# Kernel optimization log

Hardware: AMD Instinct MI355X
Metric: run time of the kernel (lower is better)

## Reference

```python
import jax, jax.numpy as jnp
import numpy as np

N = 200000   # nodes (Elliptic-scale)
E = 500000   # directed edges
F = 166      # in_channels / node feature dim
H = 128      # hidden_channels
C = 2        # out_channels
T = 49       # number of time steps


def setup_inputs() -> dict:
    key = jax.random.key(0)
    ks = jax.random.split(key, 12)
    x = jax.random.normal(ks[0], (N, F), jnp.float32)
    edge_index = jax.random.randint(ks[1], (2, E), 0, N, dtype=jnp.int32)
    time_step = jax.random.randint(ks[2], (N,), 0, T, dtype=jnp.int32)
    sF = 1.0 / np.sqrt(F)
    sH = 1.0 / np.sqrt(H)
    initial_w = jax.random.uniform(ks[3], (F, F), jnp.float32, -sF, sF)
    gru_w_ih = jax.random.uniform(ks[4], (3 * F, F), jnp.float32, -sF, sF)
    gru_w_hh = jax.random.uniform(ks[5], (3 * F, F), jnp.float32, -sF, sF)
    gru_b_ih = jax.random.uniform(ks[6], (3 * F,), jnp.float32, -sF, sF)
    gru_b_hh = jax.random.uniform(ks[7], (3 * F,), jnp.float32, -sF, sF)
    proj_w = jax.random.uniform(ks[8], (H, F), jnp.float32, -sF, sF)
    proj_b = jax.random.uniform(ks[9], (H,), jnp.float32, -sF, sF)
    cls_w = jax.random.uniform(ks[10], (C, H), jnp.float32, -sH, sH)
    cls_b = jax.random.uniform(ks[11], (C,), jnp.float32, -sH, sH)
    return {"x": x, "edge_index": edge_index, "time_step": time_step,
            "initial_w": initial_w, "gru_w_ih": gru_w_ih, "gru_w_hh": gru_w_hh,
            "gru_b_ih": gru_b_ih, "gru_b_hh": gru_b_hh,
            "proj_w": proj_w, "proj_b": proj_b, "cls_w": cls_w, "cls_b": cls_b}


def reference(x, edge_index, time_step, initial_w, gru_w_ih, gru_w_hh,
              gru_b_ih, gru_b_hh, proj_w, proj_b, cls_w, cls_b):
    src, dst = edge_index[0], edge_index[1]
    n = x.shape[0]

    def gru(W):
        # torch.nn.GRU single step, input = hidden = W  (FxF matrix, rows = batch)
        gi = W @ gru_w_ih.T + gru_b_ih
        gh = W @ gru_w_hh.T + gru_b_hh
        i_r, i_z, i_n = jnp.split(gi, 3, axis=-1)
        h_r, h_z, h_n = jnp.split(gh, 3, axis=-1)
        r = jax.nn.sigmoid(i_r + h_r)
        z = jax.nn.sigmoid(i_z + h_z)
        nn_ = jnp.tanh(i_n + r * h_n)
        return (1.0 - z) * nn_ + z * W

    def step(carry, t):
        W, logits = carry
        W = gru(W)  # evolve GCN weight (EvolveGCN-O)
        # subgraph of nodes with time_step <= t, expressed by masking (same math
        # as relabel+extract: inactive nodes contribute nothing, their outputs are ignored)
        act = time_step <= t
        ew = (act[src] & act[dst]).astype(x.dtype)
        # gcn_norm with self-loops: deg = in-degree over active edges + 1
        deg = jax.ops.segment_sum(ew, dst, num_segments=n) + 1.0
        dinv = jax.lax.rsqrt(deg)
        norm = ew * dinv[src] * dinv[dst]
        h = jnp.where(act[:, None], x, 0.0) @ W               # [N, F]
        agg = jax.ops.segment_sum(h[src] * norm[:, None], dst, num_segments=n)
        agg = agg + h / deg[:, None]                          # self-loop term dinv_i^2 * h_i
        z = jax.nn.relu(agg @ proj_w.T + proj_b)              # [N, H] (dropout: eval mode)
        lg = z @ cls_w.T + cls_b                              # [N, C]
        logits = jnp.where((time_step == t)[:, None], lg, logits)
        return (W, logits), None

    init = (initial_w, jnp.zeros((n, cls_w.shape[0]), x.dtype))
    (_, logits), _ = jax.lax.scan(step, init, jnp.arange(T, dtype=time_step.dtype))
    return logits
```

## Files before the change

### kernel.cpp

```cpp
#include <hip/hip_runtime.h>
#include <hip/hip_fp16.h>
#include <math.h>

#define NN 200000
#define NE 500000
#define FF 166
#define HH 128
#define CC 2
#define TT 49
#define GG 498
#define PADN 203136
#define MAXTILES 6400
#define KP 84
#define KPAD 192
#define SCB 512
#define SNB 391
#define HB 782
#define PREPB 420
#define CIB 1954
#define XSB 37500

typedef _Float16 half2v __attribute__((ext_vector_type(2)));
typedef _Float16 f16x4 __attribute__((ext_vector_type(4)));
typedef _Float16 f16x8 __attribute__((ext_vector_type(8)));
typedef float f32x4 __attribute__((ext_vector_type(4)));

static __device__ __forceinline__ float fdot2f(half2v a, half2v b, float c) {
#if __has_builtin(__builtin_amdgcn_fdot2)
    return __builtin_amdgcn_fdot2(a, b, c, false);
#else
    return c + (float)a.x * (float)b.x + (float)a.y * (float)b.y;
#endif
}

__global__ __launch_bounds__(256) void setup1(
        const float* __restrict__ wih, const float* __restrict__ whh,
        const float* __restrict__ projw,
        _Float16* __restrict__ wkp, float* __restrict__ projwT,
        const int* __restrict__ dstp, int* __restrict__ offc,
        const int* __restrict__ ts, int* __restrict__ cnt, int* __restrict__ rank) {
    __shared__ int h[64];
    int b = blockIdx.x;
    int tid = threadIdx.x;
    if (b < PREPB) {
        int idx = b * 256 + tid;
        const int A = 2 * KP * 512;
        if (idx < A) {
            int m = idx / (KP * 512);
            int r = idx - m * (KP * 512);
            int kp = r >> 9, c = r & 511;
            const float* Wm = m ? whh : wih;
            float x0 = 0.0f, x1 = 0.0f;
            if (c < GG) {
                int k0 = 2 * kp, k1 = 2 * kp + 1;
                if (k0 < FF) x0 = Wm[c * FF + k0];
                if (k1 < FF) x1 = Wm[c * FF + k1];
            }
            wkp[2 * idx]     = (_Float16)x0;
            wkp[2 * idx + 1] = (_Float16)x1;
        } else if (idx < A + FF * HH) {
            int q = idx - A;
            int k = q >> 7, hh = q & 127;
            projwT[q] = projw[hh * FF + k];
        }
    } else if (b < PREPB + CIB) {
        int e = (b - PREPB) * 256 + tid;
        if (e < NE) atomicAdd(&offc[dstp[e]], 1);
    } else {
        int hb = b - PREPB - CIB;
        if (tid < TT) h[tid] = 0;
        __syncthreads();
        int i = hb * 256 + tid;
        if (i < NN) {
            int t = ts[i];
            rank[i] = atomicAdd(&h[t], 1);
        }
        __syncthreads();
        if (tid < TT) cnt[hb * TT + tid] = h[tid];
    }
}

__global__ __launch_bounds__(256) void setup2(
        const int* __restrict__ off, int* __restrict__ bsum,
        const int* __restrict__ cnt, int* __restrict__ basecol, int* __restrict__ bcnt) {
    __shared__ int s[256];
    int b = blockIdx.x, tid = threadIdx.x;
    if (b < SNB) {
        int i0 = b * SCB + tid * 2;
        int v = 0;
        if (i0 < NN) v += off[i0];
        if (i0 + 1 < NN) v += off[i0 + 1];
        s[tid] = v;
        __syncthreads();
        for (int d = 128; d > 0; d >>= 1) {
            if (tid < d) s[tid] += s[tid + d];
            __syncthreads();
        }
        if (tid == 0) bsum[b] = s[0];
    } else {
        int t = b - SNB;
        const int CH = (HB + 255) / 256;
        int b0 = tid * CH;
        int loc[4];
        int sum = 0;
        for (int u = 0; u < CH; ++u) {
            int bb = b0 + u;
            int v = (bb < HB) ? cnt[bb * TT + t] : 0;
            loc[u] = sum;
            sum += v;
        }
        s[tid] = sum;
        __syncthreads();
        for (int d = 1; d < 256; d <<= 1) {
            int u = (tid >= d) ? s[tid - d] : 0;
            __syncthreads();
            s[tid] += u;
            __syncthreads();
        }
        int base = s[tid] - sum;
        for (int u = 0; u < CH; ++u) {
            int bb = b0 + u;
            if (bb < HB) basecol[bb * TT + t] = base + loc[u];
        }
        if (tid == 255) bcnt[t] = s[255];
    }
}

__global__ __launch_bounds__(512) void setup3(
        const int* __restrict__ bsum, int* __restrict__ bpre, int* __restrict__ off,
        const int* __restrict__ bcnt, int* __restrict__ pstart,
        int* __restrict__ tile_t, int* __restrict__ tile_r0, int* __restrict__ meta) {
    __shared__ int s[512];
    int tid = threadIdx.x;
    if (blockIdx.x == 0) {
        int v = (tid < SNB) ? bsum[tid] : 0;
        s[tid] = v;
        __syncthreads();
        for (int d = 1; d < 512; d <<= 1) {
            int u = (tid >= d) ? s[tid - d] : 0;
            __syncthreads();
            s[tid] += u;
            __syncthreads();
        }
        bpre[tid] = s[tid] - v;
        if (tid == 511) off[NN] = s[511];
    } else {
        int t = tid;
        int nt = (t < TT) ? (bcnt[t] + 31) / 32 : 0;
        if (t < 64) s[t] = nt;
        __syncthreads();
        for (int d = 1; d < 64; d <<= 1) {
            int v = (t >= d && t < 64) ? s[t - d] : 0;
            __syncthreads();
            if (t < 64) s[t] += v;
            __syncthreads();
        }
        if (t < 64) {
            int ntbase = s[t] - nt;
            int pbase = ntbase * 32;
            if (t < TT) {
                pstart[t] = pbase;
                for (int u = 0; u < nt; ++u) {
                    tile_t[ntbase + u] = t;
                    tile_r0[ntbase + u] = pbase + u * 32;
                }
            }
            if (t == 63) {
                meta[0] = s[63];
                meta[1] = s[63] * 32;
                pstart[TT] = s[63] * 32;
            }
        }
    }
}

__global__ __launch_bounds__(512) void setup4(
        int* __restrict__ off, const int* __restrict__ bpre,
        const int* __restrict__ ts, const int* __restrict__ rank,
        const int* __restrict__ basecol, const int* __restrict__ pstart,
        int* __restrict__ perm, int* __restrict__ pos) {
    __shared__ int s[512];
    int b = blockIdx.x, tid = threadIdx.x;
    if (b < SNB) {
        int i = b * SCB + tid;
        int v = (i < NN) ? off[i] : 0;
        s[tid] = v;
        __syncthreads();
        for (int d = 1; d < 512; d <<= 1) {
            int u = (tid >= d) ? s[tid - d] : 0;
            __syncthreads();
            s[tid] += u;
            __syncthreads();
        }
        if (i < NN) off[i] = s[tid] - v + bpre[b];
    } else {
        int i = (b - SNB) * 512 + tid;
        if (i < NN) {
            int t = ts[i];
            int hb = i >> 8;
            int p = pstart[t] + basecol[hb * TT + t] + rank[i];
            perm[p] = i;
            pos[i] = p;
        }
    }
}

__global__ __launch_bounds__(256) void setup5(
        const int* __restrict__ srcp, const int* __restrict__ dstp,
        const int* __restrict__ ts, const int* __restrict__ off,
        int* __restrict__ cursor, int2* __restrict__ adjst,
        const float* __restrict__ x, const int* __restrict__ pos,
        f16x4* __restrict__ x2p4) {
    int b = blockIdx.x, tid = threadIdx.x;
    if (b < CIB) {
        int e = b * 256 + tid;
        if (e < NE) {
            int d = dstp[e];
            int s2 = srcp[e];
            int p = atomicAdd(&cursor[d], 1);
            adjst[off[d] + p] = make_int2(s2, ts[s2]);
        }
    } else {
        int idx = (b - CIB) * 256 + tid;
        if (idx >= NN * 48) return;
        int i = idx / 48, cp4 = idx - i * 48;
        int c0 = cp4 * 4;
        float v0 = 0.f, v1 = 0.f, v2 = 0.f, v3 = 0.f;
        const float* xr = x + (size_t)i * FF;
        if (c0 + 3 < FF) {
            float2 p0 = *(const float2*)(xr + c0);
            float2 p1 = *(const float2*)(xr + c0 + 2);
            v0 = p0.x; v1 = p0.y; v2 = p1.x; v3 = p1.y;
        } else if (c0 < FF) {
            float2 p0 = *(const float2*)(xr + c0);
            v0 = p0.x; v1 = p0.y;
        }
        f16x4 h;
        h[0] = (_Float16)v0; h[1] = (_Float16)v1;
        h[2] = (_Float16)v2; h[3] = (_Float16)v3;
        x2p4[(size_t)pos[i] * 48 + cp4] = h;
    }
}

__global__ __launch_bounds__(256) void degf_hist(const int* __restrict__ off, const int2* __restrict__ adjst,
                                                 const int* __restrict__ ts, _Float16* __restrict__ dinvh,
                                                 float* __restrict__ selfdeg) {
    __shared__ unsigned short sh[TT * 256];
    int tid = threadIdx.x;
    int i = blockIdx.x * 256 + tid;
    for (int t = 0; t < TT; ++t) sh[t * 256 + tid] = 0;
    if (i >= NN) return;
    int tsi = ts[i];
    int e0 = off[i], e1 = off[i + 1];
    for (int e = e0; e < e1; ++e) {
        int tj = adjst[e].y;
        sh[tj * 256 + tid]++;
    }
    int cum = 1;
    for (int t = 0; t < TT; ++t) {
        cum += sh[t * 256 + tid];
        dinvh[(size_t)t * NN + i] = (_Float16)rsqrtf((float)cum);
        if (t == tsi) selfdeg[i] = 1.0f / (float)cum;
    }
}

__global__ __launch_bounds__(256) void edge_compact(
        const int* __restrict__ off, const int2* __restrict__ adjst,
        const int* __restrict__ ts, const _Float16* __restrict__ dinvh, const int* __restrict__ pos,
        int2* __restrict__ ewp, int* __restrict__ nact) {
    int i = blockIdx.x * 256 + threadIdx.x;
    if (i >= NN) return;
    int t = ts[i];
    const _Float16* dv = dinvh + (size_t)t * NN;
    float dvi = (float)dv[i];
    int e0 = off[i], e1 = off[i + 1];
    int c = e0;
    for (int e = e0; e < e1; ++e) {
        int2 a = adjst[e];
        if (a.y <= t) {
            float w = (float)dv[a.x] * dvi;
            ewp[c++] = make_int2(pos[a.x], __float_as_int(w));
        }
    }
    nact[i] = c - e0;
}

__global__ __launch_bounds__(512) void gru_evolve(
        const float* __restrict__ initial_w,
        const _Float16* __restrict__ wkp,
        const float* __restrict__ bih, const float* __restrict__ bhh,
        float* __restrict__ W_all) {
    __shared__ float s_w[FF];
    __shared__ __align__(16) _Float16 s_wh[2 * KP];
    __shared__ float s_pre[2][512];
    int tid = threadIdx.x;
    int row = blockIdx.x;

    if (tid < FF) {
        float v = initial_w[(size_t)row * FF + tid];
        s_w[tid] = v;
        s_wh[tid] = (_Float16)v;
    } else if (tid < 2 * KP) {
        s_wh[tid] = (_Float16)0.0f;
    }

    int cc0 = tid * 2;
    bool act = cc0 < 996;
    int m = (cc0 >= 498) ? 1 : 0;
    int c0 = act ? (cc0 - m * 498) : 0;

    half2v wr0[KP], wr1[KP];
    {
        const half2v* __restrict__ pW =
            (const half2v*)wkp + (size_t)(act ? m : 0) * (KP * 512) + c0;
        #pragma unroll
        for (int kp = 0; kp < KP; ++kp) {
            wr0[kp] = pW[(size_t)(kp << 9)];
            wr1[kp] = pW[(size_t)(kp << 9) + 1];
        }
    }

    float bi_r = 0, bi_z = 0, bi_n = 0, bh_r = 0, bh_z = 0, bh_n = 0;
    if (tid < FF) {
        bi_r = bih[tid]; bi_z = bih[FF + tid]; bi_n = bih[2 * FF + tid];
        bh_r = bhh[tid]; bh_z = bhh[FF + tid]; bh_n = bhh[2 * FF + tid];
    }
    __syncthreads();

    const f16x8* s_wh8 = (const f16x8*)s_wh;
    for (int t = 0; t < TT; ++t) {
        if (act) {
            float a0 = 0.0f, a1 = 0.0f;
            #pragma unroll
            for (int q = 0; q < 21; ++q) {
                f16x8 w8 = s_wh8[q];
                half2v h0 = __builtin_shufflevector(w8, w8, 0, 1);
                half2v h1 = __builtin_shufflevector(w8, w8, 2, 3);
                half2v h2 = __builtin_shufflevector(w8, w8, 4, 5);
                half2v h3 = __builtin_shufflevector(w8, w8, 6, 7);
                a0 = fdot2f(wr0[4 * q + 0], h0, a0);  a1 = fdot2f(wr1[4 * q + 0], h0, a1);
                a0 = fdot2f(wr0[4 * q + 1], h1, a0);  a1 = fdot2f(wr1[4 * q + 1], h1, a1);
                a0 = fdot2f(wr0[4 * q + 2], h2, a0);  a1 = fdot2f(wr1[4 * q + 2], h2, a1);
                a0 = fdot2f(wr0[4 * q + 3], h3, a0);  a1 = fdot2f(wr1[4 * q + 3], h3, a1);
            }
            s_pre[m][c0]     = a0;
            s_pre[m][c0 + 1] = a1;
        }
        __syncthreads();
        if (tid < FF) {
            float i_r = s_pre[0][tid]          + bi_r;
            float h_r = s_pre[1][tid]          + bh_r;
            float i_z = s_pre[0][FF + tid]     + bi_z;
            float h_z = s_pre[1][FF + tid]     + bh_z;
            float i_n = s_pre[0][2 * FF + tid] + bi_n;
            float h_n = s_pre[1][2 * FF + tid] + bh_n;
            float rg = 1.0f / (1.0f + expf(-(i_r + h_r)));
            float zg = 1.0f / (1.0f + expf(-(i_z + h_z)));
            float ng = tanhf(i_n + rg * h_n);
            float wnew = (1.0f - zg) * ng + zg * s_w[tid];
            s_w[tid] = wnew;
            s_wh[tid] = (_Float16)wnew;
            W_all[((size_t)t * FF + row) * FF + tid] = wnew;
        }
        __syncthreads();
    }
}

__global__ __launch_bounds__(1024) void m_build(const float* __restrict__ W_all,
                                                const float* __restrict__ projwT,
                                                _Float16* __restrict__ Mh) {
    __shared__ __align__(16) float sw[8][168];
    int blk = blockIdx.x;
    int t = blk / 24, rb = blk - t * 24;
    int tid = threadIdx.x;
    int r0 = rb * 8;
    for (int idx = tid; idx < 8 * FF; idx += 1024) {
        int rr = idx / FF, k = idx - rr * FF;
        int r = r0 + rr;
        sw[rr][k] = (r < FF) ? W_all[((size_t)t * FF + r) * FF + k] : 0.0f;
    }
    __syncthreads();
    int rr = tid >> 7, h = tid & 127;
    int r = r0 + rr;
    if (r >= KPAD) return;
    float acc = 0.0f;
    if (r < FF) {
        const float* __restrict__ pw = projwT + h;
        #pragma unroll 4
        for (int c4 = 0; c4 < 164; c4 += 4) {
            float4 w = *(const float4*)&sw[rr][c4];
            acc += w.x * pw[(size_t)(c4 + 0) << 7];
            acc += w.y * pw[(size_t)(c4 + 1) << 7];
            acc += w.z * pw[(size_t)(c4 + 2) << 7];
            acc += w.w * pw[(size_t)(c4 + 3) << 7];
        }
        acc += sw[rr][164] * pw[(size_t)164 << 7];
        acc += sw[rr][165] * pw[(size_t)165 << 7];
    }
    Mh[((size_t)t * HH + h) * KPAD + r] = (_Float16)acc;
}

__global__ __launch_bounds__(512) void gemm_fused5(
        const int* __restrict__ meta, const int* __restrict__ tile_t,
        const int* __restrict__ tile_r0, const int* __restrict__ perm,
        const float* __restrict__ selfdeg, const f16x4* __restrict__ x2p4,
        const int* __restrict__ off, const int* __restrict__ nact,
        const int2* __restrict__ ewp,
        const _Float16* __restrict__ Mh, const float* __restrict__ proj_b,
        const float* __restrict__ cls_w, const float* __restrict__ cls_b,
        float* __restrict__ out) {
    __shared__ __align__(16) char smraw[32 * 130 * 4];
    _Float16* sY = (_Float16*)smraw;
    float* sP = (float*)smraw;
    int bid = blockIdx.x;
    if (bid >= meta[0]) return;
    int t = tile_t[bid], r0 = tile_r0[bid];
    int tid = threadIdx.x;
    int lane = tid & 63;
    int w = tid >> 6;
    bool ln48 = lane < 48;

    {
        const uint4* src = (const uint4*)(x2p4 + (size_t)r0 * 48);
        #pragma unroll
        for (int u = 0; u < 2; ++u) {
            int q = tid + u * 512;
            if (q < 768) {
                int row = q / 24, kc = q - row * 24;
                *(uint4*)(sY + row * 200 + kc * 8) = src[q];
            }
        }
    }
    __syncthreads();

    int rbase = w * 4;
    int ep[4], ee[4];
    float ac[4][4];
    #pragma unroll
    for (int q = 0; q < 4; ++q) {
        int r = rbase + q;
        int i = perm[r0 + r];
        float sw = 0.0f;
        ep[q] = 0; ee[q] = 0;
        if (i >= 0) {
            sw = selfdeg[i];
            ep[q] = off[i];
            ee[q] = ep[q] + nact[i];
        }
        f16x4 h = (f16x4)((_Float16)0.0f);
        if (ln48) h = *(const f16x4*)(sY + r * 200 + lane * 4);
        ac[q][0] = sw * (float)h[0];
        ac[q][1] = sw * (float)h[1];
        ac[q][2] = sw * (float)h[2];
        ac[q][3] = sw * (float)h[3];
    }
    int2 pc[4];
    #pragma unroll
    for (int q = 0; q < 4; ++q) pc[q] = (ep[q] < ee[q]) ? ewp[ep[q]] : make_int2(0, 0);
    while ((ep[0] < ee[0]) | (ep[1] < ee[1]) | (ep[2] < ee[2]) | (ep[3] < ee[3])) {
        int js[4]; float wv[4];
        #pragma unroll
        for (int q = 0; q < 4; ++q) {
            bool val = ep[q] < ee[q];
            js[q] = pc[q].x;
            wv[q] = val ? __int_as_float(pc[q].y) : 0.0f;
            if (val) ep[q]++;
        }
        #pragma unroll
        for (int q = 0; q < 4; ++q) pc[q] = (ep[q] < ee[q]) ? ewp[ep[q]] : make_int2(0, 0);
        #pragma unroll
        for (int q = 0; q < 4; ++q) {
            if (wv[q] != 0.0f && ln48) {
                f16x4 g = x2p4[(size_t)js[q] * 48 + lane];
                ac[q][0] += wv[q] * (float)g[0];
                ac[q][1] += wv[q] * (float)g[1];
                ac[q][2] += wv[q] * (float)g[2];
                ac[q][3] += wv[q] * (float)g[3];
            }
        }
    }
    #pragma unroll
    for (int q = 0; q < 4; ++q) {
        if (ln48) {
            f16x4 o;
            o[0] = (_Float16)ac[q][0];
            o[1] = (_Float16)ac[q][1];
            o[2] = (_Float16)ac[q][2];
            o[3] = (_Float16)ac[q][3];
            *(f16x4*)(sY + (rbase + q) * 200 + lane * 4) = o;
        }
    }
    __syncthreads();

    int lr = lane & 15;
    int kg = lane >> 4;
    int c0 = w * 16;
    f32x4 acc0 = {0, 0, 0, 0}, acc1 = {0, 0, 0, 0};
    const _Float16* B0 = Mh + ((size_t)t * HH + c0 + lr) * KPAD + kg * 8;
    const _Float16* A0 = sY + lr * 200 + kg * 8;
    const _Float16* A1 = A0 + 16 * 200;

    #pragma unroll
    for (int s = 0; s < 6; ++s) {
        f16x8 b0 = *(const f16x8*)(B0 + s * 32);
        f16x8 a0 = *(const f16x8*)(A0 + s * 32);
        f16x8 a1 = *(const f16x8*)(A1 + s * 32);
        acc0 = __builtin_amdgcn_mfma_f32_16x16x32_f16(a0, b0, acc0, 0, 0, 0);
        acc1 = __builtin_amdgcn_mfma_f32_16x16x32_f16(a1, b0, acc1, 0, 0, 0);
    }

    float pb = proj_b[c0 + lr];
    __syncthreads();
    int prow = kg * 4;
    int colw = c0 + lr;
    #pragma unroll
    for (int r = 0; r < 4; ++r) {
        sP[(prow + r) * 130 + colw]      = fmaxf(acc0[r] + pb, 0.0f);
        sP[(16 + prow + r) * 130 + colw] = fmaxf(acc1[r] + pb, 0.0f);
    }
    __syncthreads();

    int row = tid >> 4, cc = (tid >> 3) & 1, qq = tid & 7;
    const float* pr = sP + row * 130 + qq * 16;
    const float* cw = cls_w + cc * HH + qq * 16;
    float s = 0.0f;
    #pragma unroll
    for (int h = 0; h < 16; ++h) s += pr[h] * cw[h];
    s += __shfl_xor(s, 1);
    s += __shfl_xor(s, 2);
    s += __shfl_xor(s, 4);
    if (qq == 0) {
        int node = perm[r0 + row];
        if (node >= 0) out[(size_t)node * CC + cc] = s + cls_b[cc];
    }
}

extern "C" void kernel_launch(void* const* d_in, const int* in_sizes, int n_in,
                              void* d_out, int out_size, void* d_ws, size_t ws_size,
                              hipStream_t stream) {
    const float* x = (const float*)d_in[0];
    const int* ei = (const int*)d_in[1];
    const int* srcp = ei;
    const int* dstp = ei + NE;
    const int* ts = (const int*)d_in[2];
    const float* initial_w = (const float*)d_in[3];
    const float* wih = (const float*)d_in[4];
    const float* whh = (const float*)d_in[5];
    const float* bih = (const float*)d_in[6];
    const float* bhh = (const float*)d_in[7];
    const float* projw = (const float*)d_in[8];
    const float* projb = (const float*)d_in[9];
    const float* clsw = (const float*)d_in[10];
    const float* clsb = (const float*)d_in[11];
    float* out = (float*)d_out;

    char* base = (char*)d_ws;
    size_t o = 0;
    auto alloc = [&](size_t bytes) { size_t r = o; o = (o + bytes + 255) & ~(size_t)255; return r; };

    float*    W_all   = (float*)   (base + alloc((size_t)TT * FF * FF * 4));
    _Float16* Mh      = (_Float16*)(base + alloc((size_t)TT * HH * KPAD * 2));
    _Float16* wkp     = (_Float16*)(base + alloc((size_t)2 * KP * 512 * 2 * 2));
    float*    projwT  = (float*)   (base + alloc((size_t)FF * HH * 4));
    int*      off     = (int*)     (base + alloc((size_t)(NN + 1) * 4));
    int*      cursor  = (int*)     (base + alloc((size_t)NN * 4));
    int2*     adjst   = (int2*)    (base + alloc((size_t)NE * 8));
    int2*     ewp     = (int2*)    (base + alloc((size_t)NE * 8));
    _Float16* dinvh   = (_Float16*)(base + alloc((size_t)TT * NN * 2));
    float*    selfdeg = (float*)   (base + alloc((size_t)NN * 4));
    int*      nact    = (int*)     (base + alloc((size_t)NN * 4));
    int*      pos     = (int*)     (base + alloc((size_t)NN * 4));
    int*      bcnt    = (int*)     (base + alloc((size_t)TT * 4));
    int*      pstart  = (int*)     (base + alloc((size_t)(TT + 1) * 4));
    int*      meta    = (int*)     (base + alloc(2 * 4));
    int*      tile_t  = (int*)     (base + alloc((size_t)MAXTILES * 4));
    int*      tile_r0 = (int*)     (base + alloc((size_t)MAXTILES * 4));
    int*      perm    = (int*)     (base + alloc((size_t)PADN * 4));
    int*      bsum    = (int*)     (base + alloc((size_t)512 * 4));
    int*      bpre    = (int*)     (base + alloc((size_t)520 * 4));
    int*      cnt     = (int*)     (base + alloc((size_t)HB * TT * 4));
    int*      basecol = (int*)     (base + alloc((size_t)HB * TT * 4));
    int*      rank    = (int*)     (base + alloc((size_t)NN * 4));
    f16x4*    x2p4    = (f16x4*)   (base + alloc((size_t)PADN * 48 * 8));

    hipMemsetAsync(off, 0, (size_t)((char*)cursor - (char*)off) + (size_t)NN * 4, stream);
    hipMemsetAsync(perm, 0xFF, (size_t)PADN * 4, stream);

    setup1<<<PREPB + CIB + HB, 256, 0, stream>>>(wih, whh, projw, wkp, projwT,
                                                 dstp, off, ts, cnt, rank);
    setup2<<<SNB + TT, 256, 0, stream>>>(off, bsum, cnt, basecol, bcnt);
    setup3<<<2, 512, 0, stream>>>(bsum, bpre, off, bcnt, pstart, tile_t, tile_r0, meta);
    setup4<<<SNB + SNB, 512, 0, stream>>>(off, bpre, ts, rank, basecol, pstart, perm, pos);
    setup5<<<CIB + XSB, 256, 0, stream>>>(srcp, dstp, ts, off, cursor, adjst, x, pos, x2p4);
    degf_hist<<<(NN + 255) / 256, 256, 0, stream>>>(off, adjst, ts, dinvh, selfdeg);
    edge_compact<<<(NN + 255) / 256, 256, 0, stream>>>(off, adjst, ts, dinvh, pos, ewp, nact);

    gru_evolve<<<FF, 512, 0, stream>>>(initial_w, wkp, bih, bhh, W_all);
    m_build<<<TT * 24, 1024, 0, stream>>>(W_all, projwT, Mh);

    gemm_fused5<<<MAXTILES, 512, 0, stream>>>(meta, tile_t, tile_r0, perm, selfdeg,
                                              x2p4, off, nact, ewp, Mh, projb, clsw, clsb, out);
}
```

Before: 334.4 us.

## Merge degree histogram with M build, pack pos into adjacency, halve GEMM block width

Several changes land at once. The degree histogram kernel and the M=W·projW build kernel are fused into one launch, and gru_evolve moves earlier in the stream. Each adjacency entry now packs the source time step and its permuted position into one int, so edge_compact no longer gathers pos. setup1 now uses 512-thread blocks. The fused GEMM kernel drops from 512 to 256 threads per tile, so each wave handles 8 rows of edge gathering and a 32x32 MFMA output block, and the edge prefetch double-buffering is removed. The goal is fewer launches and less gather traffic, at the cost of lower parallelism per tile and less latency hiding in the gather loop.

```diff
diff --git a/kernel.cpp b/kernel.cpp
--- a/kernel.cpp
+++ b/kernel.cpp
@@ -16,9 +16,13 @@
 #define SCB 512
 #define SNB 391
 #define HB 782
-#define PREPB 420
 #define CIB 1954
 #define XSB 37500
+#define P2B 210
+#define C2B 977
+#define H2B 391
+#define DEGB 782
+#define MBB (TT * 96)
 
 typedef _Float16 half2v __attribute__((ext_vector_type(2)));
 typedef _Float16 f16x4 __attribute__((ext_vector_type(4)));
@@ -33,17 +37,17 @@
 #endif
 }
 
-__global__ __launch_bounds__(256) void setup1(
+__global__ __launch_bounds__(512) void setup1(
         const float* __restrict__ wih, const float* __restrict__ whh,
         const float* __restrict__ projw,
         _Float16* __restrict__ wkp, float* __restrict__ projwT,
         const int* __restrict__ dstp, int* __restrict__ offc,
         const int* __restrict__ ts, int* __restrict__ cnt, int* __restrict__ rank) {
-    __shared__ int h[64];
+    __shared__ int h2[2][TT];
     int b = blockIdx.x;
     int tid = threadIdx.x;
-    if (b < PREPB) {
-        int idx = b * 256 + tid;
+    if (b < P2B) {
+        int idx = b * 512 + tid;
         const int A = 2 * KP * 512;
         if (idx < A) {
             int m = idx / (KP * 512);
@@ -63,226 +67,23 @@
             int k = q >> 7, hh = q & 127;
             projwT[q] = projw[hh * FF + k];
         }
-    } else if (b < PREPB + CIB) {
-        int e = (b - PREPB) * 256 + tid;
+    } else if (b < P2B + C2B) {
+        int e = (b - P2B) * 512 + tid;
         if (e < NE) atomicAdd(&offc[dstp[e]], 1);
     } else {
-        int hb = b - PREPB - CIB;
-        if (tid < TT) h[tid] = 0;
-        __syncthreads();
-        int i = hb * 256 + tid;
+        int hb2 = b - P2B - C2B;
+        int sub = tid >> 8;
+        int lt = tid & 255;
+        if (lt < TT) h2[sub][lt] = 0;
+        __syncthreads();
+        int i = hb2 * 512 + tid;
         if (i < NN) {
             int t = ts[i];
-            rank[i] = atomicAdd(&h[t], 1);
-        }
-        __syncthreads();
-        if (tid < TT) cnt[hb * TT + tid] = h[tid];
-    }
-}
-
-__global__ __launch_bounds__(256) void setup2(
-        const int* __restrict__ off, int* __restrict__ bsum,
-        const int* __restrict__ cnt, int* __restrict__ basecol, int* __restrict__ bcnt) {
-    __shared__ int s[256];
-    int b = blockIdx.x, tid = threadIdx.x;
-    if (b < SNB) {
-        int i0 = b * SCB + tid * 2;
-        int v = 0;
-        if (i0 < NN) v += off[i0];
-        if (i0 + 1 < NN) v += off[i0 + 1];
-        s[tid] = v;
-        __syncthreads();
-        for (int d = 128; d > 0; d >>= 1) {
-            if (tid < d) s[tid] += s[tid + d];
-            __syncthreads();
-        }
-        if (tid == 0) bsum[b] = s[0];
-    } else {
-        int t = b - SNB;
-        const int CH = (HB + 255) / 256;
-        int b0 = tid * CH;
-        int loc[4];
-        int sum = 0;
-        for (int u = 0; u < CH; ++u) {
-            int bb = b0 + u;
-            int v = (bb < HB) ? cnt[bb * TT + t] : 0;
-            loc[u] = sum;
-            sum += v;
-        }
-        s[tid] = sum;
-        __syncthreads();
-        for (int d = 1; d < 256; d <<= 1) {
-            int u = (tid >= d) ? s[tid - d] : 0;
-            __syncthreads();
-            s[tid] += u;
-            __syncthreads();
-        }
-        int base = s[tid] - sum;
-        for (int u = 0; u < CH; ++u) {
-            int bb = b0 + u;
-            if (bb < HB) basecol[bb * TT + t] = base + loc[u];
-        }
-        if (tid == 255) bcnt[t] = s[255];
-    }
-}
-
-__global__ __launch_bounds__(512) void setup3(
-        const int* __restrict__ bsum, int* __restrict__ bpre, int* __restrict__ off,
-        const int* __restrict__ bcnt, int* __restrict__ pstart,
-        int* __restrict__ tile_t, int* __restrict__ tile_r0, int* __restrict__ meta) {
-    __shared__ int s[512];
-    int tid = threadIdx.x;
-    if (blockIdx.x == 0) {
-        int v = (tid < SNB) ? bsum[tid] : 0;
-        s[tid] = v;
-        __syncthreads();
-        for (int d = 1; d < 512; d <<= 1) {
-            int u = (tid >= d) ? s[tid - d] : 0;
-            __syncthreads();
-            s[tid] += u;
-            __syncthreads();
-        }
-        bpre[tid] = s[tid] - v;
-        if (tid == 511) off[NN] = s[511];
-    } else {
-        int t = tid;
-        int nt = (t < TT) ? (bcnt[t] + 31) / 32 : 0;
-        if (t < 64) s[t] = nt;
-        __syncthreads();
-        for (int d = 1; d < 64; d <<= 1) {
-            int v = (t >= d && t < 64) ? s[t - d] : 0;
-            __syncthreads();
-            if (t < 64) s[t] += v;
-            __syncthreads();
-        }
-        if (t < 64) {
-            int ntbase = s[t] - nt;
-            int pbase = ntbase * 32;
-            if (t < TT) {
-                pstart[t] = pbase;
-                for (int u = 0; u < nt; ++u) {
-                    tile_t[ntbase + u] = t;
-                    tile_r0[ntbase + u] = pbase + u * 32;
-                }
-            }
-            if (t == 63) {
-                meta[0] = s[63];
-                meta[1] = s[63] * 32;
-                pstart[TT] = s[63] * 32;
-            }
-        }
-    }
-}
-
-__global__ __launch_bounds__(512) void setup4(
-        int* __restrict__ off, const int* __restrict__ bpre,
-        const int* __restrict__ ts, const int* __restrict__ rank,
-        const int* __restrict__ basecol, const int* __restrict__ pstart,
-        int* __restrict__ perm, int* __restrict__ pos) {
-    __shared__ int s[512];
-    int b = blockIdx.x, tid = threadIdx.x;
-    if (b < SNB) {
-        int i = b * SCB + tid;
-        int v = (i < NN) ? off[i] : 0;
-        s[tid] = v;
-        __syncthreads();
-        for (int d = 1; d < 512; d <<= 1) {
-            int u = (tid >= d) ? s[tid - d] : 0;
-            __syncthreads();
-            s[tid] += u;
-            __syncthreads();
-        }
-        if (i < NN) off[i] = s[tid] - v + bpre[b];
-    } else {
-        int i = (b - SNB) * 512 + tid;
-        if (i < NN) {
-            int t = ts[i];
-            int hb = i >> 8;
-            int p = pstart[t] + basecol[hb * TT + t] + rank[i];
-            perm[p] = i;
-            pos[i] = p;
-        }
-    }
-}
-
-__global__ __launch_bounds__(256) void setup5(
-        const int* __restrict__ srcp, const int* __restrict__ dstp,
-        const int* __restrict__ ts, const int* __restrict__ off,
-        int* __restrict__ cursor, int2* __restrict__ adjst,
-        const float* __restrict__ x, const int* __restrict__ pos,
-        f16x4* __restrict__ x2p4) {
-    int b = blockIdx.x, tid = threadIdx.x;
-    if (b < CIB) {
-        int e = b * 256 + tid;
-        if (e < NE) {
-            int d = dstp[e];
-            int s2 = srcp[e];
-            int p = atomicAdd(&cursor[d], 1);
-            adjst[off[d] + p] = make_int2(s2, ts[s2]);
-        }
-    } else {
-        int idx = (b - CIB) * 256 + tid;
-        if (idx >= NN * 48) return;
-        int i = idx / 48, cp4 = idx - i * 48;
-        int c0 = cp4 * 4;
-        float v0 = 0.f, v1 = 0.f, v2 = 0.f, v3 = 0.f;
-        const float* xr = x + (size_t)i * FF;
-        if (c0 + 3 < FF) {
-            float2 p0 = *(const float2*)(xr + c0);
-            float2 p1 = *(const float2*)(xr + c0 + 2);
-            v0 = p0.x; v1 = p0.y; v2 = p1.x; v3 = p1.y;
-        } else if (c0 < FF) {
-            float2 p0 = *(const float2*)(xr + c0);
-            v0 = p0.x; v1 = p0.y;
-        }
-        f16x4 h;
-        h[0] = (_Float16)v0; h[1] = (_Float16)v1;
-        h[2] = (_Float16)v2; h[3] = (_Float16)v3;
-        x2p4[(size_t)pos[i] * 48 + cp4] = h;
-    }
-}
-
-__global__ __launch_bounds__(256) void degf_hist(const int* __restrict__ off, const int2* __restrict__ adjst,
-                                                 const int* __restrict__ ts, _Float16* __restrict__ dinvh,
-                                                 float* __restrict__ selfdeg) {
-    __shared__ unsigned short sh[TT * 256];
-    int tid = threadIdx.x;
-    int i = blockIdx.x * 256 + tid;
-    for (int t = 0; t < TT; ++t) sh[t * 256 + tid] = 0;
-    if (i >= NN) return;
-    int tsi = ts[i];
-    int e0 = off[i], e1 = off[i + 1];
-    for (int e = e0; e < e1; ++e) {
-        int tj = adjst[e].y;
-        sh[tj * 256 + tid]++;
-    }
-    int cum = 1;
-    for (int t = 0; t < TT; ++t) {
-        cum += sh[t * 256 + tid];
-        dinvh[(size_t)t * NN + i] = (_Float16)rsqrtf((float)cum);
-        if (t == tsi) selfdeg[i] = 1.0f / (float)cum;
-    }
-}
-
-__global__ __launch_bounds__(256) void edge_compact(
-        const int* __restrict__ off, const int2* __restrict__ adjst,
-        const int* __restrict__ ts, const _Float16* __restrict__ dinvh, const int* __restrict__ pos,
-        int2* __restrict__ ewp, int* __restrict__ nact) {
-    int i = blockIdx.x * 256 + threadIdx.x;
-    if (i >= NN) return;
-    int t = ts[i];
-    const _Float16* dv = dinvh + (size_t)t * NN;
-    float dvi = (float)dv[i];
-    int e0 = off[i], e1 = off[i + 1];
-    int c = e0;
-    for (int e = e0; e < e1; ++e) {
-        int2 a = adjst[e];
-        if (a.y <= t) {
-            float w = (float)dv[a.x] * dvi;
-            ewp[c++] = make_int2(pos[a.x], __float_as_int(w));
-        }
-    }
-    nact[i] = c - e0;
+            rank[i] = atomicAdd(&h2[sub][t], 1);
+        }
+        __syncthreads();
+        if (lt < TT) cnt[(hb2 * 2 + sub) * TT + lt] = h2[sub][lt];
+    }
 }
 
 __global__ __launch_bounds__(512) void gru_evolve(
@@ -366,41 +167,246 @@
     }
 }
 
-__global__ __launch_bounds__(1024) void m_build(const float* __restrict__ W_all,
-                                                const float* __restrict__ projwT,
-                                                _Float16* __restrict__ Mh) {
-    __shared__ __align__(16) float sw[8][168];
-    int blk = blockIdx.x;
-    int t = blk / 24, rb = blk - t * 24;
+__global__ __launch_bounds__(256) void setup2(
+        const int* __restrict__ off, int* __restrict__ bsum,
+        const int* __restrict__ cnt, int* __restrict__ basecol, int* __restrict__ bcnt) {
+    __shared__ int s[256];
+    int b = blockIdx.x, tid = threadIdx.x;
+    if (b < SNB) {
+        int i0 = b * SCB + tid * 2;
+        int v = 0;
+        if (i0 < NN) v += off[i0];
+        if (i0 + 1 < NN) v += off[i0 + 1];
+        s[tid] = v;
+        __syncthreads();
+        for (int d = 128; d > 0; d >>= 1) {
+            if (tid < d) s[tid] += s[tid + d];
+            __syncthreads();
+        }
+        if (tid == 0) bsum[b] = s[0];
+    } else {
+        int t = b - SNB;
+        const int CH = (HB + 255) / 256;
+        int b0 = tid * CH;
+        int loc[4];
+        int sum = 0;
+        for (int u = 0; u < CH; ++u) {
+            int bb = b0 + u;
+            int v = (bb < HB) ? cnt[bb * TT + t] : 0;
+            loc[u] = sum;
+            sum += v;
+        }
+        s[tid] = sum;
+        __syncthreads();
+        for (int d = 1; d < 256; d <<= 1) {
+            int u = (tid >= d) ? s[tid - d] : 0;
+            __syncthreads();
+            s[tid] += u;
+            __syncthreads();
+        }
+        int base = s[tid] - sum;
+        for (int u = 0; u < CH; ++u) {
+            int bb = b0 + u;
+            if (bb < HB) basecol[bb * TT + t] = base + loc[u];
+        }
+        if (tid == 255) bcnt[t] = s[255];
+    }
+}
+
+__global__ __launch_bounds__(512) void setup3(
+        const int* __restrict__ bsum, int* __restrict__ bpre, int* __restrict__ off,
+        const int* __restrict__ bcnt, int* __restrict__ pstart,
+        int* __restrict__ tile_t, int* __restrict__ tile_r0, int* __restrict__ meta) {
+    __shared__ int s[512];
     int tid = threadIdx.x;
-    int r0 = rb * 8;
-    for (int idx = tid; idx < 8 * FF; idx += 1024) {
-        int rr = idx / FF, k = idx - rr * FF;
+    if (blockIdx.x == 0) {
+        int v = (tid < SNB) ? bsum[tid] : 0;
+        s[tid] = v;
+        __syncthreads();
+        for (int d = 1; d < 512; d <<= 1) {
+            int u = (tid >= d) ? s[tid - d] : 0;
+            __syncthreads();
+            s[tid] += u;
+            __syncthreads();
+        }
+        bpre[tid] = s[tid] - v;
+        if (tid == 511) off[NN] = s[511];
+    } else {
+        int t = tid;
+        int nt = (t < TT) ? (bcnt[t] + 31) / 32 : 0;
+        if (t < 64) s[t] = nt;
+        __syncthreads();
+        for (int d = 1; d < 64; d <<= 1) {
+            int v = (t >= d && t < 64) ? s[t - d] : 0;
+            __syncthreads();
+            if (t < 64) s[t] += v;
+            __syncthreads();
+        }
+        if (t < 64) {
+            int ntbase = s[t] - nt;
+            int pbase = ntbase * 32;
+            if (t < TT) {
+                pstart[t] = pbase;
+                for (int u = 0; u < nt; ++u) {
+                    tile_t[ntbase + u] = t;
+                    tile_r0[ntbase + u] = pbase + u * 32;
+                }
+            }
+            if (t == 63) {
+                meta[0] = s[63];
+                meta[1] = s[63] * 32;
+                pstart[TT] = s[63] * 32;
+            }
+        }
+    }
+}
+
+__global__ __launch_bounds__(512) void setup4(
+        int* __restrict__ off, const int* __restrict__ bpre,
+        const int* __restrict__ ts, const int* __restrict__ rank,
+        const int* __restrict__ basecol, const int* __restrict__ pstart,
+        int* __restrict__ perm, int* __restrict__ pos) {
+    __shared__ int s[512];
+    int b = blockIdx.x, tid = threadIdx.x;
+    if (b < SNB) {
+        int i = b * SCB + tid;
+        int v = (i < NN) ? off[i] : 0;
+        s[tid] = v;
+        __syncthreads();
+        for (int d = 1; d < 512; d <<= 1) {
+            int u = (tid >= d) ? s[tid - d] : 0;
+            __syncthreads();
+            s[tid] += u;
+            __syncthreads();
+        }
+        if (i < NN) off[i] = s[tid] - v + bpre[b];
+    } else {
+        int i = (b - SNB) * 512 + tid;
+        if (i < NN) {
+            int t = ts[i];
+            int hb = i >> 8;
+            int p = pstart[t] + basecol[hb * TT + t] + rank[i];
+            perm[p] = i;
+            pos[i] = p;
+        }
+    }
+}
+
+__global__ __launch_bounds__(256) void setup5(
+        const int* __restrict__ srcp, const int* __restrict__ dstp,
+        const int* __restrict__ ts, const int* __restrict__ off,
+        int* __restrict__ cursor, int2* __restrict__ adjst,
+        const float* __restrict__ x, const int* __restrict__ pos,
+        f16x4* __restrict__ x2p4) {
+    int b = blockIdx.x, tid = threadIdx.x;
+    if (b < CIB) {
+        int e = b * 256 + tid;
+        if (e < NE) {
+            int d = dstp[e];
+            int s2 = srcp[e];
+            int p = atomicAdd(&cursor[d], 1);
+            adjst[off[d] + p] = make_int2(s2, (ts[s2] << 25) | pos[s2]);
+        }
+    } else {
+        int idx = (b - CIB) * 256 + tid;
+        if (idx >= NN * 48) return;
+        int i = idx / 48, cp4 = idx - i * 48;
+        int c0 = cp4 * 4;
+        float v0 = 0.f, v1 = 0.f, v2 = 0.f, v3 = 0.f;
+        const float* xr = x + (size_t)i * FF;
+        if (c0 + 3 < FF) {
+            float2 p0 = *(const float2*)(xr + c0);
+            float2 p1 = *(const float2*)(xr + c0 + 2);
+            v0 = p0.x; v1 = p0.y; v2 = p1.x; v3 = p1.y;
+        } else if (c0 < FF) {
+            float2 p0 = *(const float2*)(xr + c0);
+            v0 = p0.x; v1 = p0.y;
+        }
+        f16x4 h;
+        h[0] = (_Float16)v0; h[1] = (_Float16)v1;
+        h[2] = (_Float16)v2; h[3] = (_Float16)v3;
+        x2p4[(size_t)pos[i] * 48 + cp4] = h;
+    }
+}
+
+__global__ __launch_bounds__(256) void degf_m(
+        const int* __restrict__ off, const int2* __restrict__ adjst,
+        const int* __restrict__ ts, _Float16* __restrict__ dinvh,
+        float* __restrict__ selfdeg,
+        const float* __restrict__ W_all, const float* __restrict__ projwT,
+        _Float16* __restrict__ Mh) {
+    __shared__ unsigned short sh[TT * 256];
+    __shared__ __align__(16) float sw2[2][168];
+    int b = blockIdx.x;
+    int tid = threadIdx.x;
+    if (b < DEGB) {
+        int i = b * 256 + tid;
+        for (int t = 0; t < TT; ++t) sh[t * 256 + tid] = 0;
+        if (i >= NN) return;
+        int tsi = ts[i];
+        int e0 = off[i], e1 = off[i + 1];
+        for (int e = e0; e < e1; ++e) {
+            int tj = adjst[e].y >> 25;
+            sh[tj * 256 + tid]++;
+        }
+        int cum = 1;
+        for (int t = 0; t < TT; ++t) {
+            cum += sh[t * 256 + tid];
+            dinvh[(size_t)t * NN + i] = (_Float16)rsqrtf((float)cum);
+            if (t == tsi) selfdeg[i] = 1.0f / (float)cum;
+        }
+    } else {
+        int mb = b - DEGB;
+        int t = mb / 96, rb = mb - t * 96;
+        int r0 = rb * 2;
+        for (int idx = tid; idx < 2 * FF; idx += 256) {
+            int rr = idx / FF, k = idx - rr * FF;
+            int r = r0 + rr;
+            sw2[rr][k] = (r < FF) ? W_all[((size_t)t * FF + r) * FF + k] : 0.0f;
+        }
+        __syncthreads();
+        int rr = tid >> 7, h = tid & 127;
         int r = r0 + rr;
-        sw[rr][k] = (r < FF) ? W_all[((size_t)t * FF + r) * FF + k] : 0.0f;
-    }
-    __syncthreads();
-    int rr = tid >> 7, h = tid & 127;
-    int r = r0 + rr;
-    if (r >= KPAD) return;
-    float acc = 0.0f;
-    if (r < FF) {
-        const float* __restrict__ pw = projwT + h;
-        #pragma unroll 4
-        for (int c4 = 0; c4 < 164; c4 += 4) {
-            float4 w = *(const float4*)&sw[rr][c4];
-            acc += w.x * pw[(size_t)(c4 + 0) << 7];
-            acc += w.y * pw[(size_t)(c4 + 1) << 7];
-            acc += w.z * pw[(size_t)(c4 + 2) << 7];
-            acc += w.w * pw[(size_t)(c4 + 3) << 7];
-        }
-        acc += sw[rr][164] * pw[(size_t)164 << 7];
-        acc += sw[rr][165] * pw[(size_t)165 << 7];
-    }
-    Mh[((size_t)t * HH + h) * KPAD + r] = (_Float16)acc;
-}
-
-__global__ __launch_bounds__(512) void gemm_fused5(
+        float acc = 0.0f;
+        if (r < FF) {
+            const float* __restrict__ pw = projwT + h;
+            #pragma unroll 4
+            for (int c4 = 0; c4 < 164; c4 += 4) {
+                float4 w = *(const float4*)&sw2[rr][c4];
+                acc += w.x * pw[(size_t)(c4 + 0) << 7];
+                acc += w.y * pw[(size_t)(c4 + 1) << 7];
+                acc += w.z * pw[(size_t)(c4 + 2) << 7];
+                acc += w.w * pw[(size_t)(c4 + 3) << 7];
+            }
+            acc += sw2[rr][164] * pw[(size_t)164 << 7];
+            acc += sw2[rr][165] * pw[(size_t)165 << 7];
+        }
+        Mh[((size_t)t * HH + h) * KPAD + r] = (_Float16)acc;
+    }
+}
+
+__global__ __launch_bounds__(256) void edge_compact(
+        const int* __restrict__ off, const int2* __restrict__ adjst,
+        const int* __restrict__ ts, const _Float16* __restrict__ dinvh,
+        int2* __restrict__ ewp, int* __restrict__ nact) {
+    int i = blockIdx.x * 256 + threadIdx.x;
+    if (i >= NN) return;
+    int t = ts[i];
+    const _Float16* dv = dinvh + (size_t)t * NN;
+    float dvi = (float)dv[i];
+    int e0 = off[i], e1 = off[i + 1];
+    int c = e0;
+    for (int e = e0; e < e1; ++e) {
+        int2 a = adjst[e];
+        if ((a.y >> 25) <= t) {
+            float w = (float)dv[a.x] * dvi;
+            ewp[c++] = make_int2(a.y & 0x1FFFFFF, __float_as_int(w));
+        }
+    }
+    nact[i] = c - e0;
+}
+
+__global__ __launch_bounds__(256) void gemm_fused6(
         const int* __restrict__ meta, const int* __restrict__ tile_t,
         const int* __restrict__ tile_r0, const int* __restrict__ perm,
         const float* __restrict__ selfdeg, const f16x4* __restrict__ x2p4,
@@ -423,21 +429,19 @@
     {
         const uint4* src = (const uint4*)(x2p4 + (size_t)r0 * 48);
         #pragma unroll
-        for (int u = 0; u < 2; ++u) {
-            int q = tid + u * 512;
-            if (q < 768) {
-                int row = q / 24, kc = q - row * 24;
-                *(uint4*)(sY + row * 200 + kc * 8) = src[q];
-            }
+        for (int u = 0; u < 3; ++u) {
+            int q = tid + u * 256;
+            int row = q / 24, kc = q - row * 24;
+            *(uint4*)(sY + row * 200 + kc * 8) = src[q];
         }
     }
     __syncthreads();
 
-    int rbase = w * 4;
-    int ep[4], ee[4];
-    float ac[4][4];
+    int rbase = w * 8;
+    int ep[8], ee[8];
+    float ac[8][4];
     #pragma unroll
-    for (int q = 0; q < 4; ++q) {
+    for (int q = 0; q < 8; ++q) {
         int r = rbase + q;
         int i = perm[r0 + r];
         float sw = 0.0f;
@@ -454,22 +458,21 @@
         ac[q][2] = sw * (float)h[2];
         ac[q][3] = sw * (float)h[3];
     }
-    int2 pc[4];
+    bool more = false;
     #pragma unroll
-    for (int q = 0; q < 4; ++q) pc[q] = (ep[q] < ee[q]) ? ewp[ep[q]] : make_int2(0, 0);
-    while ((ep[0] < ee[0]) | (ep[1] < ee[1]) | (ep[2] < ee[2]) | (ep[3] < ee[3])) {
-        int js[4]; float wv[4];
+    for (int q = 0; q < 8; ++q) more |= (ep[q] < ee[q]);
+    while (more) {
+        int js[8]; float wv[8];
         #pragma unroll
-        for (int q = 0; q < 4; ++q) {
-            bool val = ep[q] < ee[q];
-            js[q] = pc[q].x;
-            wv[q] = val ? __int_as_float(pc[q].y) : 0.0f;
-            if (val) ep[q]++;
+        for (int q = 0; q < 8; ++q) {
+            bool v = ep[q] < ee[q];
+            int2 p = v ? ewp[ep[q]] : make_int2(0, 0);
+            js[q] = p.x;
+            wv[q] = v ? __int_as_float(p.y) : 0.0f;
+            if (v) ep[q]++;
         }
         #pragma unroll
-        for (int q = 0; q < 4; ++q) pc[q] = (ep[q] < ee[q]) ? ewp[ep[q]] : make_int2(0, 0);
-        #pragma unroll
-        for (int q = 0; q < 4; ++q) {
+        for (int q = 0; q < 8; ++q) {
             if (wv[q] != 0.0f && ln48) {
                 f16x4 g = x2p4[(size_t)js[q] * 48 + lane];
                 ac[q][0] += wv[q] * (float)g[0];
@@ -478,9 +481,12 @@
                 ac[q][3] += wv[q] * (float)g[3];
             }
         }
+        more = false;
+        #pragma unroll
+        for (int q = 0; q < 8; ++q) more |= (ep[q] < ee[q]);
     }
     #pragma unroll
-    for (int q = 0; q < 4; ++q) {
+    for (int q = 0; q < 8; ++q) {
         if (ln48) {
             f16x4 o;
             o[0] = (_Float16)ac[q][0];
@@ -494,41 +500,46 @@
 
     int lr = lane & 15;
     int kg = lane >> 4;
-    int c0 = w * 16;
-    f32x4 acc0 = {0, 0, 0, 0}, acc1 = {0, 0, 0, 0};
-    const _Float16* B0 = Mh + ((size_t)t * HH + c0 + lr) * KPAD + kg * 8;
+    f32x4 acc00 = {0,0,0,0}, acc01 = {0,0,0,0}, acc10 = {0,0,0,0}, acc11 = {0,0,0,0};
+    const _Float16* B0 = Mh + ((size_t)t * HH + w * 32 + lr) * KPAD + kg * 8;
+    const _Float16* B1 = B0 + 16 * KPAD;
     const _Float16* A0 = sY + lr * 200 + kg * 8;
     const _Float16* A1 = A0 + 16 * 200;
 
     #pragma unroll
     for (int s = 0; s < 6; ++s) {
-        f16x8 b0 = *(const f16x8*)(B0 + s * 32);
         f16x8 a0 = *(const f16x8*)(A0 + s * 32);
         f16x8 a1 = *(const f16x8*)(A1 + s * 32);
-        acc0 = __builtin_amdgcn_mfma_f32_16x16x32_f16(a0, b0, acc0, 0, 0, 0);
-        acc1 = __builtin_amdgcn_mfma_f32_16x16x32_f16(a1, b0, acc1, 0, 0, 0);
-    }
-
-    float pb = proj_b[c0 + lr];
+        f16x8 b0 = *(const f16x8*)(B0 + s * 32);
+        f16x8 b1 = *(const f16x8*)(B1 + s * 32);
+        acc00 = __builtin_amdgcn_mfma_f32_16x16x32_f16(a0, b0, acc00, 0, 0, 0);
+        acc01 = __builtin_amdgcn_mfma_f32_16x16x32_f16(a0, b1, acc01, 0, 0, 0);
+        acc10 = __builtin_amdgcn_mfma_f32_16x16x32_f16(a1, b0, acc10, 0, 0, 0);
+        acc11 = __builtin_amdgcn_mfma_f32_16x16x32_f16(a1, b1, acc11, 0, 0, 0);
+    }
+
+    float pb0 = proj_b[w * 32 + lr];
+    float pb1 = proj_b[w * 32 + 16 + lr];
     __syncthreads();
     int prow = kg * 4;
-    int colw = c0 + lr;
+    int col0 = w * 32 + lr;
     #pragma unroll
     for (int r = 0; r < 4; ++r) {
-        sP[(prow + r) * 130 + colw]      = fmaxf(acc0[r] + pb, 0.0f);
-        sP[(16 + prow + r) * 130 + colw] = fmaxf(acc1[r] + pb, 0.0f);
+        sP[(prow + r) * 130 + col0]           = fmaxf(acc00[r] + pb0, 0.0f);
+        sP[(prow + r) * 130 + col0 + 16]      = fmaxf(acc01[r] + pb1, 0.0f);
+        sP[(16 + prow + r) * 130 + col0]      = fmaxf(acc10[r] + pb0, 0.0f);
+        sP[(16 + prow + r) * 130 + col0 + 16] = fmaxf(acc11[r] + pb1, 0.0f);
     }
     __syncthreads();
 
-    int row = tid >> 4, cc = (tid >> 3) & 1, qq = tid & 7;
-    const float* pr = sP + row * 130 + qq * 16;
-    const float* cw = cls_w + cc * HH + qq * 16;
+    int row = tid >> 3, cc = (tid >> 2) & 1, qq = tid & 3;
+    const float* pr = sP + row * 130 + qq * 32;
+    const float* cw = cls_w + cc * HH + qq * 32;
     float s = 0.0f;
-    #pragma unroll
-    for (int h = 0; h < 16; ++h) s += pr[h] * cw[h];
+    #pragma unroll 8
+    for (int h = 0; h < 32; ++h) s += pr[h] * cw[h];
     s += __shfl_xor(s, 1);
     s += __shfl_xor(s, 2);
-    s += __shfl_xor(s, 4);
     if (qq == 0) {
         int node = perm[r0 + row];
         if (node >= 0) out[(size_t)node * CC + cc] = s + cls_b[cc];
@@ -586,18 +597,16 @@
     hipMemsetAsync(off, 0, (size_t)((char*)cursor - (char*)off) + (size_t)NN * 4, stream);
     hipMemsetAsync(perm, 0xFF, (size_t)PADN * 4, stream);
 
-    setup1<<<PREPB + CIB + HB, 256, 0, stream>>>(wih, whh, projw, wkp, projwT,
-                                                 dstp, off, ts, cnt, rank);
+    setup1<<<P2B + C2B + H2B, 512, 0, stream>>>(wih, whh, projw, wkp, projwT,
+                                                dstp, off, ts, cnt, rank);
+    gru_evolve<<<FF, 512, 0, stream>>>(initial_w, wkp, bih, bhh, W_all);
     setup2<<<SNB + TT, 256, 0, stream>>>(off, bsum, cnt, basecol, bcnt);
     setup3<<<2, 512, 0, stream>>>(bsum, bpre, off, bcnt, pstart, tile_t, tile_r0, meta);
     setup4<<<SNB + SNB, 512, 0, stream>>>(off, bpre, ts, rank, basecol, pstart, perm, pos);
     setup5<<<CIB + XSB, 256, 0, stream>>>(srcp, dstp, ts, off, cursor, adjst, x, pos, x2p4);
-    degf_hist<<<(NN + 255) / 256, 256, 0, stream>>>(off, adjst, ts, dinvh, selfdeg);
-    edge_compact<<<(NN + 255) / 256, 256, 0, stream>>>(off, adjst, ts, dinvh, pos, ewp, nact);
-
-    gru_evolve<<<FF, 512, 0, stream>>>(initial_w, wkp, bih, bhh, W_all);
-    m_build<<<TT * 24, 1024, 0, stream>>>(W_all, projwT, Mh);
-
-    gemm_fused5<<<MAXTILES, 512, 0, stream>>>(meta, tile_t, tile_r0, perm, selfdeg,
+    degf_m<<<DEGB + MBB, 256, 0, stream>>>(off, adjst, ts, dinvh, selfdeg, W_all, projwT, Mh);
+    edge_compact<<<(NN + 255) / 256, 256, 0, stream>>>(off, adjst, ts, dinvh, ewp, nact);
+
+    gemm_fused6<<<MAXTILES, 256, 0, stream>>>(meta, tile_t, tile_r0, perm, selfdeg,
                                               x2p4, off, nact, ewp, Mh, projb, clsw, clsb, out);
 }
```

New measurement: 369.9 us. 10.6% more time.
